# Performance work log

Hardware: AMD Instinct MI355X
Metric: run time of the kernel (lower is better)

## Reference

```python
import jax, jax.numpy as jnp
import numpy as np

N_NODES = 100000
N_EDGES = 3200000
N_RELS = 8
F_IN = 64
F_OUT = 64


def setup_inputs() -> dict:
    key = jax.random.key(0)
    k1, k2, k3, k4, k5, k6 = jax.random.split(key, 6)
    X = jax.random.normal(k1, (N_NODES, F_IN), dtype=jnp.float32)
    W = jax.random.normal(k2, (N_RELS, F_IN, F_OUT), dtype=jnp.float32) * 0.1
    A = jax.random.uniform(k3, (N_EDGES,), dtype=jnp.float32)
    src = jax.random.randint(k4, (N_EDGES,), 0, N_NODES, dtype=jnp.int32)
    dst = jax.random.randint(k5, (N_EDGES,), 0, N_NODES, dtype=jnp.int32)
    etype = jax.random.randint(k6, (N_EDGES,), 0, N_RELS, dtype=jnp.int32)
    return {"X": X, "W": W, "A": A, "src": src, "dst": dst, "etype": etype}


def reference(X, W, A, src, dst, etype):
    # RGCN hetero forward: Y[i,fo] = sum_{r,j in N_r(i)} A[r,i,j] * (X[j] @ W[r])[fo]
    # Precompute per-relation transformed features: [R, N, F_out]
    XW = jnp.einsum('nf,rfo->rno', X, W)
    # Gather per-edge message and scale by edge weight: [E, F_out]
    msg = XW[etype, src] * A[:, None]
    # Scatter-add into destination nodes: [N, F_out]
    Y = jax.ops.segment_sum(msg, dst, num_segments=X.shape[0])
    return Y
```

## Files before the change

### kernel.cpp

```cpp
#include <hip/hip_runtime.h>
#include <hip/hip_fp16.h>

#define FDIM 64
#define SB 200
#define P_BLK 1024
#define NB_MAX 400
#define BKT_NODES 256
#define CHUNK_CAP 3200

typedef __attribute__((ext_vector_type(8))) short short8;
typedef __attribute__((ext_vector_type(4))) float float4_;

__device__ __forceinline__ unsigned short f2bf(float x) {
    unsigned u = __float_as_uint(x);
    return (unsigned short)((u + 0x7FFF + ((u >> 16) & 1)) >> 16);
}

__global__ __launch_bounds__(256) void xw_gemm_mfma(
    const float* __restrict__ X, const float* __restrict__ Wmat,
    __half* __restrict__ XWh, int N, int R)
{
    __shared__ unsigned short Wt[4 * 64 * 72];
    const int tid  = threadIdx.x;
    const int lane = tid & 63;
    const int wave = tid >> 6;
    const int quad = lane >> 4;
    const int l15  = lane & 15;
    const int blockBase = blockIdx.x * 256;

    short8 bfrag[4][2];
    bool tvalid[4];
#pragma unroll
    for (int t = 0; t < 4; ++t) {
        const int tb = blockBase + (wave * 4 + t) * 16;
        tvalid[t] = (tb < N);
        if (tvalid[t]) {
            const float* xp = X + (size_t)(tb + l15) * FDIM + quad * 8;
            const float4 x0 = *(const float4*)(xp);
            const float4 x1 = *(const float4*)(xp + 4);
            const float4 x2 = *(const float4*)(xp + 32);
            const float4 x3 = *(const float4*)(xp + 36);
            short8 b0, b1;
            b0[0]=f2bf(x0.x); b0[1]=f2bf(x0.y); b0[2]=f2bf(x0.z); b0[3]=f2bf(x0.w);
            b0[4]=f2bf(x1.x); b0[5]=f2bf(x1.y); b0[6]=f2bf(x1.z); b0[7]=f2bf(x1.w);
            b1[0]=f2bf(x2.x); b1[1]=f2bf(x2.y); b1[2]=f2bf(x2.z); b1[3]=f2bf(x2.w);
            b1[4]=f2bf(x3.x); b1[5]=f2bf(x3.y); b1[6]=f2bf(x3.z); b1[7]=f2bf(x3.w);
            bfrag[t][0] = b0; bfrag[t][1] = b1;
        } else {
            bfrag[t][0] = (short8)(0); bfrag[t][1] = (short8)(0);
        }
    }

    for (int rp = 0; rp < 2; ++rp) {
        __syncthreads();
#pragma unroll
        for (int it = 0; it < 16; ++it) {
            const int idx = it * 256 + tid;
            const int k  = idx & 63;
            const int f4 = (idx >> 6) & 15;
            const int r  = idx >> 10;
            const float4 w = *(const float4*)(Wmat + (((size_t)(rp * 4 + r) * FDIM + k) * FDIM + f4 * 4));
            const int base = (r * 64 + f4 * 4) * 72 + k;
            Wt[base + 0 * 72] = f2bf(w.x);
            Wt[base + 1 * 72] = f2bf(w.y);
            Wt[base + 2 * 72] = f2bf(w.z);
            Wt[base + 3 * 72] = f2bf(w.w);
        }
        __syncthreads();

#pragma unroll
        for (int t = 0; t < 4; ++t) {
            if (!tvalid[t]) continue;
            const int tb = blockBase + (wave * 4 + t) * 16;
            const int node = tb + l15;
#pragma unroll
            for (int r = 0; r < 4; ++r) {
                __half* orow = XWh + ((size_t)(rp * 4 + r) * N + node) * FDIM;
#pragma unroll
                for (int ft = 0; ft < 4; ++ft) {
                    const int f = ft * 16 + l15;
                    const unsigned short* wp = &Wt[(r * 64 + f) * 72 + quad * 8];
                    const short8 a0 = *(const short8*)(wp);
                    const short8 a1 = *(const short8*)(wp + 32);
                    float4_ acc = {0.f, 0.f, 0.f, 0.f};
                    acc = __builtin_amdgcn_mfma_f32_16x16x32_bf16(a0, bfrag[t][0], acc, 0, 0, 0);
                    acc = __builtin_amdgcn_mfma_f32_16x16x32_bf16(a1, bfrag[t][1], acc, 0, 0, 0);
                    const __half2 h01 = __floats2half2_rn(acc[0], acc[1]);
                    const __half2 h23 = __floats2half2_rn(acc[2], acc[3]);
                    uint2 st;
                    st.x = *(const unsigned*)&h01;
                    st.y = *(const unsigned*)&h23;
                    *(uint2*)(orow + ft * 16 + quad * 4) = st;
                }
            }
        }
    }
}

__global__ __launch_bounds__(256) void bin_hist(
    const int* __restrict__ dst, int* __restrict__ cnt, int E, int B, int chunk)
{
    __shared__ int lh[NB_MAX];
    const int p = blockIdx.x, tid = threadIdx.x;
    for (int b = tid; b < B; b += 256) lh[b] = 0;
    __syncthreads();
    const int i0 = p * chunk, iend = min(i0 + chunk, E);
    for (int i = i0 + tid; i < iend; i += 256)
        atomicAdd(&lh[dst[i] >> 8], 1);
    __syncthreads();
    for (int b = tid; b < B; b += 256) cnt[(size_t)b * P_BLK + p] = lh[b];
}

__global__ __launch_bounds__(256) void scan_partial(
    const int* __restrict__ cnt, int* __restrict__ blockSums, int M, int CH)
{
    __shared__ int sh[256];
    const int b = blockIdx.x, tid = threadIdx.x;
    const int i0 = b * CH, iend = min(i0 + CH, M);
    int s = 0;
    for (int i = i0 + tid; i < iend; i += 256) s += cnt[i];
    sh[tid] = s; __syncthreads();
    for (int off = 128; off > 0; off >>= 1) {
        if (tid < off) sh[tid] += sh[tid + off];
        __syncthreads();
    }
    if (tid == 0) blockSums[b] = sh[0];
}

__global__ __launch_bounds__(256) void scan_block(int* blockSums, int nb)
{
    __shared__ int sh[256];
    const int tid = threadIdx.x;
    const int v = (tid < nb) ? blockSums[tid] : 0;
    sh[tid] = v; __syncthreads();
    for (int off = 1; off < 256; off <<= 1) {
        const int t = (tid >= off) ? sh[tid - off] : 0;
        __syncthreads();
        sh[tid] += t;
        __syncthreads();
    }
    if (tid < nb) blockSums[tid] = sh[tid] - v;
}

__global__ __launch_bounds__(64) void scan_final(
    const int* __restrict__ cnt, const int* __restrict__ blockSums,
    int* __restrict__ offs, int M, int CH, int E)
{
    const int b = blockIdx.x, lane = threadIdx.x;
    const int i0 = b * CH, iend = min(i0 + CH, M);
    int carry = blockSums[b];
    for (int t = i0; t < iend; t += 64) {
        const int i = t + lane;
        const int c = (i < iend) ? cnt[i] : 0;
        int v = c;
#pragma unroll
        for (int o = 1; o < 64; o <<= 1) {
            const int u = __shfl_up(v, o, 64);
            if (lane >= o) v += u;
        }
        if (i < iend) offs[i] = carry + v - c;
        carry += __shfl(v, 63, 64);
    }
    if (b == (int)gridDim.x - 1 && lane == 0) offs[M] = E;
}

__global__ __launch_bounds__(256) void bin_scatter(
    const int* __restrict__ src, const int* __restrict__ dst,
    const int* __restrict__ etype, const float* __restrict__ A,
    const int* __restrict__ offs, int2* __restrict__ packed,
    int E, int N, int B, int chunk)
{
    __shared__ int lcnt[NB_MAX];
    __shared__ int lpfx[NB_MAX];
    __shared__ int gb[NB_MAX];
    __shared__ int2 recs[CHUNK_CAP];
    __shared__ unsigned short rbkt[CHUNK_CAP];
    const int p = blockIdx.x, tid = threadIdx.x;
    const int i0 = p * chunk, iend = min(i0 + chunk, E);

    for (int b = tid; b < B; b += 256) lcnt[b] = 0;
    __syncthreads();
    for (int i = i0 + tid; i < iend; i += 256)
        atomicAdd(&lcnt[dst[i] >> 8], 1);
    __syncthreads();

    if (tid < 64) {
        int carry = 0;
        for (int t0 = 0; t0 < B; t0 += 64) {
            const int b = t0 + tid;
            const int c = (b < B) ? lcnt[b] : 0;
            int v = c;
#pragma unroll
            for (int o = 1; o < 64; o <<= 1) {
                const int u = __shfl_up(v, o, 64);
                if (tid >= o) v += u;
            }
            if (b < B) lpfx[b] = carry + v - c;
            carry += __shfl(v, 63, 64);
        }
    }
    __syncthreads();
    for (int b = tid; b < B; b += 256) {
        gb[b] = offs[(size_t)b * P_BLK + p] - lpfx[b];
        lcnt[b] = lpfx[b];
    }
    __syncthreads();

    for (int i = i0 + tid; i < iend; i += 256) {
        const int d = dst[i];
        const int b = d >> 8;
        const int slot = atomicAdd(&lcnt[b], 1);
        recs[slot] = make_int2((etype[i] * N + src[i]) | ((d & 255) << 20),
                               __float_as_int(A[i]));
        rbkt[slot] = (unsigned short)b;
    }
    __syncthreads();

    const int tot = iend - i0;
    for (int s = tid; s < tot; s += 256)
        packed[gb[rbkt[s]] + s] = recs[s];
}

__global__ __launch_bounds__(1024) void bucket_sort(
    const int2* __restrict__ packed, const int* __restrict__ offs,
    int2* __restrict__ sorted, int* __restrict__ nodeOffs, int N, int B, int E)
{
    __shared__ int hist[BKT_NODES];
    __shared__ int pfx[BKT_NODES + 1];
    __shared__ int cur[BKT_NODES];
    const int bkt = blockIdx.x, tid = threadIdx.x;
    const int beg = offs[(size_t)bkt * P_BLK];
    const int end = (bkt + 1 < B) ? offs[(size_t)(bkt + 1) * P_BLK] : E;

    if (tid < BKT_NODES) hist[tid] = 0;
    __syncthreads();
    for (int i = beg + tid; i < end; i += 1024)
        atomicAdd(&hist[(packed[i].x >> 20) & (BKT_NODES - 1)], 1);
    __syncthreads();
    if (tid == 0) {
        int s = 0;
        pfx[0] = 0;
        for (int i = 0; i < BKT_NODES; ++i) { s += hist[i]; pfx[i + 1] = s; }
    }
    __syncthreads();
    if (tid < BKT_NODES) {
        cur[tid] = pfx[tid];
        const int n = bkt * BKT_NODES + tid;
        if (n < N) nodeOffs[n] = beg + pfx[tid];
    }
    if (bkt == B - 1 && tid == 0) nodeOffs[N] = E;
    __syncthreads();
    for (int i = beg + tid; i < end; i += 1024) {
        const int2 rec = packed[i];
        const int dl = (rec.x >> 20) & (BKT_NODES - 1);
        const int pos = atomicAdd(&cur[dl], 1);
        sorted[beg + pos] = rec;
    }
}

__global__ __launch_bounds__(256) void dst_aggregate(
    const __half* __restrict__ XWh, const int* __restrict__ nodeOffs,
    const int2* __restrict__ sorted, float* __restrict__ Y, int N)
{
    const int lane = threadIdx.x & 63;
    const int hid  = lane >> 5;
    const int fl   = lane & 31;
    const int wave = (int)((blockIdx.x * blockDim.x + threadIdx.x) >> 6);
    const int nWaves = (int)((gridDim.x * blockDim.x) >> 6);
    const __half2* XW2 = (const __half2*)XWh;

    for (int d = wave; d < N; d += nWaves) {
        const int beg = nodeOffs[d], end = nodeOffs[d + 1];
        float ax = 0.f, ay = 0.f;
        for (int base = beg; base < end; base += 64) {
            const int idx = base + lane;
            const int2 ka = (idx < end) ? sorted[idx] : make_int2(0, 0);
            const int nb = min(64, end - base);
            const int npair = (nb + 1) >> 1;
            int s = 0;
            for (; s + 8 <= npair; s += 8) {
                int k[8], b[8];
#pragma unroll
                for (int u = 0; u < 8; ++u) {
                    const int j = 2 * (s + u) + hid;
                    k[u] = __shfl(ka.x, j, 64);
                    b[u] = __shfl(ka.y, j, 64);
                }
                __half2 v[8];
#pragma unroll
                for (int u = 0; u < 8; ++u)
                    v[u] = XW2[(size_t)(k[u] & 0xFFFFF) * 32 + fl];
#pragma unroll
                for (int u = 0; u < 8; ++u) {
                    const float2 f = __half22float2(v[u]);
                    const float a = __int_as_float(b[u]);
                    ax += a * f.x; ay += a * f.y;
                }
            }
            for (; s < npair; ++s) {
                const int j = 2 * s + hid;
                const int kk = __shfl(ka.x, j, 64);
                const int bb = __shfl(ka.y, j, 64);
                const __half2 v = XW2[(size_t)(kk & 0xFFFFF) * 32 + fl];
                const float2 f = __half22float2(v);
                const float a = __int_as_float(bb);
                ax += a * f.x; ay += a * f.y;
            }
        }
        ax += __shfl_xor(ax, 32, 64);
        ay += __shfl_xor(ay, 32, 64);
        if (lane < 32) {
            ((float2*)(Y + (size_t)d * FDIM))[fl] = make_float2(ax, ay);
        }
    }
}

extern "C" void kernel_launch(void* const* d_in, const int* in_sizes, int n_in,
                              void* d_out, int out_size, void* d_ws, size_t ws_size,
                              hipStream_t stream)
{
    const float* X     = (const float*)d_in[0];
    const float* Wmat  = (const float*)d_in[1];
    const float* A     = (const float*)d_in[2];
    const int*   src   = (const int*)d_in[3];
    const int*   dst   = (const int*)d_in[4];
    const int*   etype = (const int*)d_in[5];
    float* Y = (float*)d_out;

    const int N = in_sizes[0] / FDIM;
    const int R = in_sizes[1] / (FDIM * FDIM);
    const int E = in_sizes[2];
    (void)n_in; (void)out_size; (void)ws_size;

    const int B = (N + BKT_NODES - 1) / BKT_NODES;
    const int M = B * P_BLK;
    const int chunk = (E + P_BLK - 1) / P_BLK;
    const int CH = (M + SB - 1) / SB;

    char* ws = (char*)d_ws;
    size_t off = 0;
    auto take = [&](size_t bytes) { char* p = ws + off; off = (off + bytes + 255) & ~(size_t)255; return p; };
    __half* XWh      = (__half*)take((size_t)R * N * FDIM * sizeof(__half));
    int2*   packed   = (int2*)  take((size_t)E * sizeof(int2));
    int2*   sorted   = (int2*)  take((size_t)E * sizeof(int2));
    int*    cnt      = (int*)   take((size_t)M * sizeof(int));
    int*    offs     = (int*)   take((size_t)(M + 1) * sizeof(int));
    int*    nodeOffs = (int*)   take((size_t)(N + 1) * sizeof(int));
    int*    bsums    = (int*)   take((size_t)SB * sizeof(int));

    xw_gemm_mfma<<<(N + 255) / 256, 256, 0, stream>>>(X, Wmat, XWh, N, R);

    bin_hist<<<P_BLK, 256, 0, stream>>>(dst, cnt, E, B, chunk);
    scan_partial<<<SB, 256, 0, stream>>>(cnt, bsums, M, CH);
    scan_block<<<1, 256, 0, stream>>>(bsums, SB);
    scan_final<<<SB, 64, 0, stream>>>(cnt, bsums, offs, M, CH, E);
    bin_scatter<<<P_BLK, 256, 0, stream>>>(src, dst, etype, A, offs, packed, E, N, B, chunk);
    bucket_sort<<<B, 1024, 0, stream>>>(packed, offs, sorted, nodeOffs, N, B, E);

    dst_aggregate<<<2048, 256, 0, stream>>>(XWh, nodeOffs, sorted, Y, N);
}
```

Baseline: 315.0 us.

## Widen aggregation gathers to 8-byte loads and halve GEMM block tile

The destination aggregation kernel now has each wave process four edges per step, with 16 lanes per edge each loading 4 halves (uint2) instead of two edges with 32 lanes loading half2. This gives fewer, wider gather instructions and fewer loop iterations, at the cost of one more cross-lane reduction step at the end. The XW GEMM kernel also handles 128 nodes per block instead of 256, which doubles the grid size. That should improve occupancy and load balance but repeats the per-block W staging twice as often.

```diff
diff --git a/kernel.cpp b/kernel.cpp
--- a/kernel.cpp
+++ b/kernel.cpp
@@ -26,13 +26,13 @@
     const int wave = tid >> 6;
     const int quad = lane >> 4;
     const int l15  = lane & 15;
-    const int blockBase = blockIdx.x * 256;
-
-    short8 bfrag[4][2];
-    bool tvalid[4];
-#pragma unroll
-    for (int t = 0; t < 4; ++t) {
-        const int tb = blockBase + (wave * 4 + t) * 16;
+    const int blockBase = blockIdx.x * 128;
+
+    short8 bfrag[2][2];
+    bool tvalid[2];
+#pragma unroll
+    for (int t = 0; t < 2; ++t) {
+        const int tb = blockBase + (wave * 2 + t) * 16;
         tvalid[t] = (tb < N);
         if (tvalid[t]) {
             const float* xp = X + (size_t)(tb + l15) * FDIM + quad * 8;
@@ -69,9 +69,9 @@
         __syncthreads();
 
 #pragma unroll
-        for (int t = 0; t < 4; ++t) {
+        for (int t = 0; t < 2; ++t) {
             if (!tvalid[t]) continue;
-            const int tb = blockBase + (wave * 4 + t) * 16;
+            const int tb = blockBase + (wave * 2 + t) * 16;
             const int node = tb + l15;
 #pragma unroll
             for (int r = 0; r < 4; ++r) {
@@ -263,54 +263,60 @@
     const int2* __restrict__ sorted, float* __restrict__ Y, int N)
 {
     const int lane = threadIdx.x & 63;
-    const int hid  = lane >> 5;
-    const int fl   = lane & 31;
+    const int hid  = lane >> 4;
+    const int fl   = lane & 15;
     const int wave = (int)((blockIdx.x * blockDim.x + threadIdx.x) >> 6);
     const int nWaves = (int)((gridDim.x * blockDim.x) >> 6);
-    const __half2* XW2 = (const __half2*)XWh;
+    const uint2* XW4 = (const uint2*)XWh;
 
     for (int d = wave; d < N; d += nWaves) {
         const int beg = nodeOffs[d], end = nodeOffs[d + 1];
-        float ax = 0.f, ay = 0.f;
+        float ax = 0.f, ay = 0.f, az = 0.f, aw = 0.f;
         for (int base = beg; base < end; base += 64) {
             const int idx = base + lane;
             const int2 ka = (idx < end) ? sorted[idx] : make_int2(0, 0);
             const int nb = min(64, end - base);
-            const int npair = (nb + 1) >> 1;
+            const int nquad = (nb + 3) >> 2;
             int s = 0;
-            for (; s + 8 <= npair; s += 8) {
+            for (; s + 8 <= nquad; s += 8) {
                 int k[8], b[8];
 #pragma unroll
                 for (int u = 0; u < 8; ++u) {
-                    const int j = 2 * (s + u) + hid;
+                    const int j = 4 * (s + u) + hid;
                     k[u] = __shfl(ka.x, j, 64);
                     b[u] = __shfl(ka.y, j, 64);
                 }
-                __half2 v[8];
+                uint2 v[8];
 #pragma unroll
                 for (int u = 0; u < 8; ++u)
-                    v[u] = XW2[(size_t)(k[u] & 0xFFFFF) * 32 + fl];
+                    v[u] = XW4[(size_t)(k[u] & 0xFFFFF) * 16 + fl];
 #pragma unroll
                 for (int u = 0; u < 8; ++u) {
-                    const float2 f = __half22float2(v[u]);
+                    const float2 f01 = __half22float2(*(const __half2*)&v[u].x);
+                    const float2 f23 = __half22float2(*(const __half2*)&v[u].y);
                     const float a = __int_as_float(b[u]);
-                    ax += a * f.x; ay += a * f.y;
+                    ax += a * f01.x; ay += a * f01.y;
+                    az += a * f23.x; aw += a * f23.y;
                 }
             }
-            for (; s < npair; ++s) {
-                const int j = 2 * s + hid;
+            for (; s < nquad; ++s) {
+                const int j = 4 * s + hid;
                 const int kk = __shfl(ka.x, j, 64);
                 const int bb = __shfl(ka.y, j, 64);
-                const __half2 v = XW2[(size_t)(kk & 0xFFFFF) * 32 + fl];
-                const float2 f = __half22float2(v);
+                const uint2 v = XW4[(size_t)(kk & 0xFFFFF) * 16 + fl];
+                const float2 f01 = __half22float2(*(const __half2*)&v.x);
+                const float2 f23 = __half22float2(*(const __half2*)&v.y);
                 const float a = __int_as_float(bb);
-                ax += a * f.x; ay += a * f.y;
+                ax += a * f01.x; ay += a * f01.y;
+                az += a * f23.x; aw += a * f23.y;
             }
         }
-        ax += __shfl_xor(ax, 32, 64);
-        ay += __shfl_xor(ay, 32, 64);
-        if (lane < 32) {
-            ((float2*)(Y + (size_t)d * FDIM))[fl] = make_float2(ax, ay);
+        ax += __shfl_xor(ax, 16, 64); ay += __shfl_xor(ay, 16, 64);
+        az += __shfl_xor(az, 16, 64); aw += __shfl_xor(aw, 16, 64);
+        ax += __shfl_xor(ax, 32, 64); ay += __shfl_xor(ay, 32, 64);
+        az += __shfl_xor(az, 32, 64); aw += __shfl_xor(aw, 32, 64);
+        if (lane < 16) {
+            ((float4*)(Y + (size_t)d * FDIM))[fl] = make_float4(ax, ay, az, aw);
         }
     }
 }
@@ -348,7 +354,7 @@
     int*    nodeOffs = (int*)   take((size_t)(N + 1) * sizeof(int));
     int*    bsums    = (int*)   take((size_t)SB * sizeof(int));
 
-    xw_gemm_mfma<<<(N + 255) / 256, 256, 0, stream>>>(X, Wmat, XWh, N, R);
+    xw_gemm_mfma<<<(N + 127) / 128, 256, 0, stream>>>(X, Wmat, XWh, N, R);
 
     bin_hist<<<P_BLK, 256, 0, stream>>>(dst, cnt, E, B, chunk);
     scan_partial<<<SB, 256, 0, stream>>>(cnt, bsums, M, CH);
```

After: 328.7 us. 1.04x slower.
